# Performance work log

Measured on AMD Instinct MI355X. Metric: run time of the kernel, lower is better.

Reference implementation:

```python
import jax, jax.numpy as jnp
import numpy as np

TAU = 0.05
SIGMA = 0.05
THETA = 1.0
MAX_ITER = 30
B, N, M1, M2 = 8192, 256, 128, 64


def setup_inputs() -> dict:
    key = jax.random.key(0)
    k = jax.random.split(key, 5)
    x0 = jax.random.normal(k[0], (B, N), dtype=jnp.float32)
    y1_0 = jnp.zeros((B, M1), dtype=jnp.float32)
    y2_0 = jnp.zeros((B, M2), dtype=jnp.float32)
    z = jax.random.normal(k[1], (B, M1 + M2), dtype=jnp.float32)
    c = jax.random.normal(k[2], (N,), dtype=jnp.float32)
    # scale constraint matrices so tau*sigma*||A||^2 < 1 (PDHG stability)
    A1 = jax.random.normal(k[3], (M1, N), dtype=jnp.float32) * 0.1
    A2 = jax.random.normal(k[4], (M2, N), dtype=jnp.float32) * 0.1
    return {"x0": x0, "y1_0": y1_0, "y2_0": y2_0, "z": z, "c": c, "A1": A1, "A2": A2}


def reference(x0, y1_0, y2_0, z, c, A1, A2):
    # affine constraint maps: ineq_map(x, z) = x @ A1^T - z1 ; eq_map(x, z) = x @ A2^T - z2
    # adjoints: A1^T y1 = y1 @ A1 ; A2^T y2 = y2 @ A2
    # prox: projection onto nonnegative orthant
    z1, z2 = z[:, :M1], z[:, M1:]

    def step(carry, _):
        x, x_bar, y1, y2 = carry
        y1 = jnp.maximum(y1 + SIGMA * (x_bar @ A1.T - z1), 0.0)   # dual ineq ascent + clamp
        y2 = y2 + SIGMA * (x_bar @ A2.T - z2)                     # dual eq ascent
        grad = c + y1 @ A1 + y2 @ A2                              # [B, N] via broadcast of c
        x_next = jnp.maximum(x - TAU * grad, 0.0)                 # prox (nonneg projection)
        x_bar = x_next + THETA * (x_next - x)                     # extrapolation
        return (x_next, x_bar, y1, y2), None

    (x, _, y1, y2), _ = jax.lax.scan(step, (x0, x0, y1_0, y2_0), None, length=MAX_ITER)
    return (x, y1, y2)
```

## Files before the change

kernel.cpp:

```cpp
#include <hip/hip_runtime.h>

typedef __attribute__((ext_vector_type(8))) __bf16 bf16x8;
typedef __attribute__((ext_vector_type(4))) float f32x4;
typedef __attribute__((ext_vector_type(4))) int i32x4;

constexpr int Bn = 8192, Nn = 256, M1n = 128, M2n = 64, Mn = 192, ITERS = 30;
constexpr float TAUc = 0.05f, SIGc = 0.05f;

__device__ __forceinline__ ushort f2bf(float f) {
  unsigned u = __builtin_bit_cast(unsigned, f);
  u = (u + 0x7FFFu + ((u >> 16) & 1u)) >> 16;
  return (ushort)u;
}

__device__ __forceinline__ unsigned cvtpk(float lo, float hi) {
  unsigned r;
  asm("v_cvt_pk_bf16_f32 %0, %1, %2" : "=v"(r) : "v"(lo), "v"(hi));
  return r;
}

__device__ __forceinline__ void pina(i32x4& v) { asm volatile("" : "+a"(v)); }

__device__ __forceinline__ f32x4 mfma_swp(i32x4 afrag, bf16x8 b, f32x4 acc) {
  return __builtin_amdgcn_mfma_f32_16x16x32_bf16(
      __builtin_bit_cast(bf16x8, afrag), b, acc, 0, 0, 0);
}

__global__ void prep_kernel(const float* __restrict__ A1, const float* __restrict__ A2,
                            ushort* __restrict__ Arm, ushort* __restrict__ AT) {
  int i = blockIdx.x * 256 + threadIdx.x;
  if (i >= Mn * Nn) return;
  int m = i / Nn, n = i % Nn;
  float v = (m < M1n) ? A1[m * Nn + n] : A2[(m - M1n) * Nn + n];
  ushort b = f2bf(v);
  Arm[m * Nn + n] = b;
  AT[n * Mn + m] = b;
}

__global__ __launch_bounds__(512, 2) void pdhg_kernel(
    const float* __restrict__ x0, const float* __restrict__ y10,
    const float* __restrict__ y20, const float* __restrict__ z,
    const float* __restrict__ c, const ushort* __restrict__ Arm,
    const ushort* __restrict__ AT, float* __restrict__ out) {
  __shared__ __align__(16) ushort xb_lds[2][16][264];
  __shared__ __align__(16) ushort y_lds[2][16][200];

  const int lane = threadIdx.x & 63;
  const int w = threadIdx.x >> 6;
  const int fr = lane & 15;
  const int kg = lane >> 4;
  const int row0 = blockIdx.x * 32;

  const int b1 = w & 1;
  const int mg = w >> 1;
  const int rG1 = row0 + 16 * b1 + fr;

  float x[2][2][4];
  float cv[2][4];
  float ys[3][4], zs[3][4];

#pragma unroll
  for (int t = 0; t < 2; ++t) {
    const int n0 = (2 * w + t) * 16 + kg * 4;
    *reinterpret_cast<f32x4*>(cv[t]) = *reinterpret_cast<const f32x4*>(&c[n0]);
#pragma unroll
    for (int b = 0; b < 2; ++b) {
      f32x4 v = *reinterpret_cast<const f32x4*>(&x0[(row0 + 16 * b + fr) * Nn + n0]);
#pragma unroll
      for (int g = 0; g < 4; ++g) x[t][b][g] = v[g];
      uint2 p = make_uint2(cvtpk(v[0], v[1]), cvtpk(v[2], v[3]));
      *reinterpret_cast<uint2*>(&xb_lds[b][fr][n0]) = p;
    }
  }
#pragma unroll
  for (int i = 0; i < 3; ++i) {
    const int mt = 3 * mg + i;
    const int m0 = mt * 16 + kg * 4;
    f32x4 zv = *reinterpret_cast<const f32x4*>(&z[rG1 * Mn + m0]);
    f32x4 yv = (mt < 8) ? *reinterpret_cast<const f32x4*>(&y10[rG1 * M1n + m0])
                        : *reinterpret_cast<const f32x4*>(&y20[rG1 * M2n + (m0 - M1n)]);
#pragma unroll
    for (int g = 0; g < 4; ++g) { zs[i][g] = SIGc * zv[g]; ys[i][g] = yv[g]; }
  }

  i32x4 armF[3][8], atF[2][6];
#pragma unroll
  for (int i = 0; i < 3; ++i) {
    const int m = (3 * mg + i) * 16 + fr;
#pragma unroll
    for (int kf = 0; kf < 8; ++kf) {
      armF[i][kf] = *reinterpret_cast<const i32x4*>(&Arm[m * Nn + kf * 32 + kg * 8]);
      pina(armF[i][kf]);
    }
  }
#pragma unroll
  for (int t = 0; t < 2; ++t) {
    const int n = (2 * w + t) * 16 + fr;
#pragma unroll
    for (int kf = 0; kf < 6; ++kf) {
      atF[t][kf] = *reinterpret_cast<const i32x4*>(&AT[n * Mn + kf * 32 + kg * 8]);
      pina(atF[t][kf]);
    }
  }

  __syncthreads();

  for (int it = 0; it < ITERS; ++it) {
    f32x4 a0 = {0.f, 0.f, 0.f, 0.f}, a1 = a0, a2 = a0;
#pragma unroll
    for (int kf = 0; kf < 8; ++kf) {
      bf16x8 fx = *reinterpret_cast<const bf16x8*>(&xb_lds[b1][fr][kf * 32 + kg * 8]);
      a0 = mfma_swp(armF[0][kf], fx, a0);
      a1 = mfma_swp(armF[1][kf], fx, a1);
      a2 = mfma_swp(armF[2][kf], fx, a2);
    }

#pragma unroll
    for (int i = 0; i < 3; ++i) {
      const int mt = 3 * mg + i;
      const int m0 = mt * 16 + kg * 4;
      const f32x4 ai = (i == 0) ? a0 : (i == 1) ? a1 : a2;
      const bool relu = (mt < 8);
#pragma unroll
      for (int g = 0; g < 4; ++g) {
        float s = __builtin_fmaf(SIGc, ai[g], ys[i][g]) - zs[i][g];
        ys[i][g] = relu ? fmaxf(s, 0.f) : s;
      }
      uint2 p = make_uint2(cvtpk(ys[i][0], ys[i][1]), cvtpk(ys[i][2], ys[i][3]));
      *reinterpret_cast<uint2*>(&y_lds[b1][fr][m0]) = p;
    }
    __syncthreads();

    f32x4 q00 = {0.f, 0.f, 0.f, 0.f}, q01 = q00, q10 = q00, q11 = q00;
#pragma unroll
    for (int kf = 0; kf < 6; ++kf) {
      bf16x8 g0 = *reinterpret_cast<const bf16x8*>(&y_lds[0][fr][kf * 32 + kg * 8]);
      bf16x8 g1 = *reinterpret_cast<const bf16x8*>(&y_lds[1][fr][kf * 32 + kg * 8]);
      q00 = mfma_swp(atF[0][kf], g0, q00);
      q01 = mfma_swp(atF[1][kf], g0, q01);
      q10 = mfma_swp(atF[0][kf], g1, q10);
      q11 = mfma_swp(atF[1][kf], g1, q11);
    }

    const bool notlast = (it != ITERS - 1);
#pragma unroll
    for (int t = 0; t < 2; ++t) {
      const int n0 = (2 * w + t) * 16 + kg * 4;
#pragma unroll
      for (int b = 0; b < 2; ++b) {
        const f32x4 qt = (t == 0) ? (b == 0 ? q00 : q10) : (b == 0 ? q01 : q11);
        float xb[4];
#pragma unroll
        for (int g = 0; g < 4; ++g) {
          float grad = cv[t][g] + qt[g];
          float xn = fmaxf(__builtin_fmaf(-TAUc, grad, x[t][b][g]), 0.f);
          xb[g] = 2.f * xn - x[t][b][g];
          x[t][b][g] = xn;
        }
        if (notlast) {
          uint2 p = make_uint2(cvtpk(xb[0], xb[1]), cvtpk(xb[2], xb[3]));
          *reinterpret_cast<uint2*>(&xb_lds[b][fr][n0]) = p;
        }
      }
    }
    if (notlast) __syncthreads();
  }

  float* ox = out;
  float* oy1 = out + Bn * Nn;
  float* oy2 = oy1 + Bn * M1n;
#pragma unroll
  for (int t = 0; t < 2; ++t) {
    const int n0 = (2 * w + t) * 16 + kg * 4;
#pragma unroll
    for (int b = 0; b < 2; ++b) {
      f32x4 v;
#pragma unroll
      for (int g = 0; g < 4; ++g) v[g] = x[t][b][g];
      *reinterpret_cast<f32x4*>(&ox[(row0 + 16 * b + fr) * Nn + n0]) = v;
    }
  }
#pragma unroll
  for (int i = 0; i < 3; ++i) {
    const int mt = 3 * mg + i;
    const int m0 = mt * 16 + kg * 4;
    f32x4 v;
#pragma unroll
    for (int g = 0; g < 4; ++g) v[g] = ys[i][g];
    if (mt < 8) *reinterpret_cast<f32x4*>(&oy1[rG1 * M1n + m0]) = v;
    else        *reinterpret_cast<f32x4*>(&oy2[rG1 * M2n + (m0 - M1n)]) = v;
  }
}

extern "C" void kernel_launch(void* const* d_in, const int* in_sizes, int n_in,
                              void* d_out, int out_size, void* d_ws, size_t ws_size,
                              hipStream_t stream) {
  const float* x0  = (const float*)d_in[0];
  const float* y10 = (const float*)d_in[1];
  const float* y20 = (const float*)d_in[2];
  const float* z   = (const float*)d_in[3];
  const float* c   = (const float*)d_in[4];
  const float* A1  = (const float*)d_in[5];
  const float* A2  = (const float*)d_in[6];

  ushort* Arm = (ushort*)d_ws;
  ushort* AT  = Arm + Mn * Nn;

  prep_kernel<<<(Mn * Nn + 255) / 256, 256, 0, stream>>>(A1, A2, Arm, AT);
  pdhg_kernel<<<Bn / 32, 512, 0, stream>>>(x0, y10, y20, z, c, Arm, AT, (float*)d_out);
}
```

Before: 67.69 us.

## Shrink PDHG blocks to 16 rows with 4 waves each

```diff
diff --git a/kernel.cpp b/kernel.cpp
--- a/kernel.cpp
+++ b/kernel.cpp
@@ -37,56 +37,50 @@
   AT[n * Mn + m] = b;
 }
 
-__global__ __launch_bounds__(512, 2) void pdhg_kernel(
+__global__ __launch_bounds__(256, 2) void pdhg_kernel(
     const float* __restrict__ x0, const float* __restrict__ y10,
     const float* __restrict__ y20, const float* __restrict__ z,
     const float* __restrict__ c, const ushort* __restrict__ Arm,
     const ushort* __restrict__ AT, float* __restrict__ out) {
-  __shared__ __align__(16) ushort xb_lds[2][16][264];
-  __shared__ __align__(16) ushort y_lds[2][16][200];
+  __shared__ __align__(16) ushort xb_lds[16][264];
+  __shared__ __align__(16) ushort y_lds[16][200];
 
   const int lane = threadIdx.x & 63;
   const int w = threadIdx.x >> 6;
   const int fr = lane & 15;
   const int kg = lane >> 4;
-  const int row0 = blockIdx.x * 32;
+  const int row0 = blockIdx.x * 16;
+  const int rG = row0 + fr;
 
-  const int b1 = w & 1;
-  const int mg = w >> 1;
-  const int rG1 = row0 + 16 * b1 + fr;
-
-  float x[2][2][4];
-  float cv[2][4];
+  float x[4][4];
+  float cv[4][4];
   float ys[3][4], zs[3][4];
 
 #pragma unroll
-  for (int t = 0; t < 2; ++t) {
-    const int n0 = (2 * w + t) * 16 + kg * 4;
+  for (int t = 0; t < 4; ++t) {
+    const int n0 = (4 * w + t) * 16 + kg * 4;
     *reinterpret_cast<f32x4*>(cv[t]) = *reinterpret_cast<const f32x4*>(&c[n0]);
+    f32x4 v = *reinterpret_cast<const f32x4*>(&x0[rG * Nn + n0]);
 #pragma unroll
-    for (int b = 0; b < 2; ++b) {
-      f32x4 v = *reinterpret_cast<const f32x4*>(&x0[(row0 + 16 * b + fr) * Nn + n0]);
-#pragma unroll
-      for (int g = 0; g < 4; ++g) x[t][b][g] = v[g];
-      uint2 p = make_uint2(cvtpk(v[0], v[1]), cvtpk(v[2], v[3]));
-      *reinterpret_cast<uint2*>(&xb_lds[b][fr][n0]) = p;
-    }
+    for (int g = 0; g < 4; ++g) x[t][g] = v[g];
+    uint2 p = make_uint2(cvtpk(v[0], v[1]), cvtpk(v[2], v[3]));
+    *reinterpret_cast<uint2*>(&xb_lds[fr][n0]) = p;
   }
 #pragma unroll
   for (int i = 0; i < 3; ++i) {
-    const int mt = 3 * mg + i;
+    const int mt = 3 * w + i;
     const int m0 = mt * 16 + kg * 4;
-    f32x4 zv = *reinterpret_cast<const f32x4*>(&z[rG1 * Mn + m0]);
-    f32x4 yv = (mt < 8) ? *reinterpret_cast<const f32x4*>(&y10[rG1 * M1n + m0])
-                        : *reinterpret_cast<const f32x4*>(&y20[rG1 * M2n + (m0 - M1n)]);
+    f32x4 zv = *reinterpret_cast<const f32x4*>(&z[rG * Mn + m0]);
+    f32x4 yv = (mt < 8) ? *reinterpret_cast<const f32x4*>(&y10[rG * M1n + m0])
+                        : *reinterpret_cast<const f32x4*>(&y20[rG * M2n + (m0 - M1n)]);
 #pragma unroll
     for (int g = 0; g < 4; ++g) { zs[i][g] = SIGc * zv[g]; ys[i][g] = yv[g]; }
   }
 
-  i32x4 armF[3][8], atF[2][6];
+  i32x4 armF[3][8], atF[4][6];
 #pragma unroll
   for (int i = 0; i < 3; ++i) {
-    const int m = (3 * mg + i) * 16 + fr;
+    const int m = (3 * w + i) * 16 + fr;
 #pragma unroll
     for (int kf = 0; kf < 8; ++kf) {
       armF[i][kf] = *reinterpret_cast<const i32x4*>(&Arm[m * Nn + kf * 32 + kg * 8]);
@@ -94,8 +88,8 @@
     }
   }
 #pragma unroll
-  for (int t = 0; t < 2; ++t) {
-    const int n = (2 * w + t) * 16 + fr;
+  for (int t = 0; t < 4; ++t) {
+    const int n = (4 * w + t) * 16 + fr;
 #pragma unroll
     for (int kf = 0; kf < 6; ++kf) {
       atF[t][kf] = *reinterpret_cast<const i32x4*>(&AT[n * Mn + kf * 32 + kg * 8]);
@@ -109,7 +103,7 @@
     f32x4 a0 = {0.f, 0.f, 0.f, 0.f}, a1 = a0, a2 = a0;
 #pragma unroll
     for (int kf = 0; kf < 8; ++kf) {
-      bf16x8 fx = *reinterpret_cast<const bf16x8*>(&xb_lds[b1][fr][kf * 32 + kg * 8]);
+      bf16x8 fx = *reinterpret_cast<const bf16x8*>(&xb_lds[fr][kf * 32 + kg * 8]);
       a0 = mfma_swp(armF[0][kf], fx, a0);
       a1 = mfma_swp(armF[1][kf], fx, a1);
       a2 = mfma_swp(armF[2][kf], fx, a2);
@@ -117,7 +111,7 @@
 
 #pragma unroll
     for (int i = 0; i < 3; ++i) {
-      const int mt = 3 * mg + i;
+      const int mt = 3 * w + i;
       const int m0 = mt * 16 + kg * 4;
       const f32x4 ai = (i == 0) ? a0 : (i == 1) ? a1 : a2;
       const bool relu = (mt < 8);
@@ -127,40 +121,36 @@
         ys[i][g] = relu ? fmaxf(s, 0.f) : s;
       }
       uint2 p = make_uint2(cvtpk(ys[i][0], ys[i][1]), cvtpk(ys[i][2], ys[i][3]));
-      *reinterpret_cast<uint2*>(&y_lds[b1][fr][m0]) = p;
+      *reinterpret_cast<uint2*>(&y_lds[fr][m0]) = p;
     }
     __syncthreads();
 
-    f32x4 q00 = {0.f, 0.f, 0.f, 0.f}, q01 = q00, q10 = q00, q11 = q00;
+    f32x4 q0 = {0.f, 0.f, 0.f, 0.f}, q1 = q0, q2 = q0, q3 = q0;
 #pragma unroll
     for (int kf = 0; kf < 6; ++kf) {
-      bf16x8 g0 = *reinterpret_cast<const bf16x8*>(&y_lds[0][fr][kf * 32 + kg * 8]);
-      bf16x8 g1 = *reinterpret_cast<const bf16x8*>(&y_lds[1][fr][kf * 32 + kg * 8]);
-      q00 = mfma_swp(atF[0][kf], g0, q00);
-      q01 = mfma_swp(atF[1][kf], g0, q01);
-      q10 = mfma_swp(atF[0][kf], g1, q10);
-      q11 = mfma_swp(atF[1][kf], g1, q11);
+      bf16x8 fy = *reinterpret_cast<const bf16x8*>(&y_lds[fr][kf * 32 + kg * 8]);
+      q0 = mfma_swp(atF[0][kf], fy, q0);
+      q1 = mfma_swp(atF[1][kf], fy, q1);
+      q2 = mfma_swp(atF[2][kf], fy, q2);
+      q3 = mfma_swp(atF[3][kf], fy, q3);
     }
 
     const bool notlast = (it != ITERS - 1);
 #pragma unroll
-    for (int t = 0; t < 2; ++t) {
-      const int n0 = (2 * w + t) * 16 + kg * 4;
+    for (int t = 0; t < 4; ++t) {
+      const int n0 = (4 * w + t) * 16 + kg * 4;
+      const f32x4 qt = (t == 0) ? q0 : (t == 1) ? q1 : (t == 2) ? q2 : q3;
+      float xb[4];
 #pragma unroll
-      for (int b = 0; b < 2; ++b) {
-        const f32x4 qt = (t == 0) ? (b == 0 ? q00 : q10) : (b == 0 ? q01 : q11);
-        float xb[4];
-#pragma unroll
-        for (int g = 0; g < 4; ++g) {
-          float grad = cv[t][g] + qt[g];
-          float xn = fmaxf(__builtin_fmaf(-TAUc, grad, x[t][b][g]), 0.f);
-          xb[g] = 2.f * xn - x[t][b][g];
-          x[t][b][g] = xn;
-        }
-        if (notlast) {
-          uint2 p = make_uint2(cvtpk(xb[0], xb[1]), cvtpk(xb[2], xb[3]));
-          *reinterpret_cast<uint2*>(&xb_lds[b][fr][n0]) = p;
-        }
+      for (int g = 0; g < 4; ++g) {
+        float grad = cv[t][g] + qt[g];
+        float xn = fmaxf(__builtin_fmaf(-TAUc, grad, x[t][g]), 0.f);
+        xb[g] = 2.f * xn - x[t][g];
+        x[t][g] = xn;
+      }
+      if (notlast) {
+        uint2 p = make_uint2(cvtpk(xb[0], xb[1]), cvtpk(xb[2], xb[3]));
+        *reinterpret_cast<uint2*>(&xb_lds[fr][n0]) = p;
       }
     }
     if (notlast) __syncthreads();
@@ -170,25 +160,22 @@
   float* oy1 = out + Bn * Nn;
   float* oy2 = oy1 + Bn * M1n;
 #pragma unroll
-  for (int t = 0; t < 2; ++t) {
-    const int n0 = (2 * w + t) * 16 + kg * 4;
+  for (int t = 0; t < 4; ++t) {
+    const int n0 = (4 * w + t) * 16 + kg * 4;
+    f32x4 v;
 #pragma unroll
-    for (int b = 0; b < 2; ++b) {
-      f32x4 v;
-#pragma unroll
-      for (int g = 0; g < 4; ++g) v[g] = x[t][b][g];
-      *reinterpret_cast<f32x4*>(&ox[(row0 + 16 * b + fr) * Nn + n0]) = v;
-    }
+    for (int g = 0; g < 4; ++g) v[g] = x[t][g];
+    *reinterpret_cast<f32x4*>(&ox[rG * Nn + n0]) = v;
   }
 #pragma unroll
   for (int i = 0; i < 3; ++i) {
-    const int mt = 3 * mg + i;
+    const int mt = 3 * w + i;
     const int m0 = mt * 16 + kg * 4;
     f32x4 v;
 #pragma unroll
     for (int g = 0; g < 4; ++g) v[g] = ys[i][g];
-    if (mt < 8) *reinterpret_cast<f32x4*>(&oy1[rG1 * M1n + m0]) = v;
-    else        *reinterpret_cast<f32x4*>(&oy2[rG1 * M2n + (m0 - M1n)]) = v;
+    if (mt < 8) *reinterpret_cast<f32x4*>(&oy1[rG * M1n + m0]) = v;
+    else        *reinterpret_cast<f32x4*>(&oy2[rG * M2n + (m0 - M1n)]) = v;
   }
 }
 
@@ -207,5 +194,5 @@
   ushort* AT  = Arm + Mn * Nn;
 
   prep_kernel<<<(Mn * Nn + 255) / 256, 256, 0, stream>>>(A1, A2, Arm, AT);
-  pdhg_kernel<<<Bn / 32, 512, 0, stream>>>(x0, y10, y20, z, c, Arm, AT, (float*)d_out);
+  pdhg_kernel<<<Bn / 16, 256, 0, stream>>>(x0, y10, y20, z, c, Arm, AT, (float*)d_out);
 }
```

After: 102.2 us. 1.51x slower.

## Software-pipeline the two 16-row halves so dual and primal GEMMs overlap

Applied to the files above, without the earlier changes.

```diff
diff --git a/kernel.cpp b/kernel.cpp
--- a/kernel.cpp
+++ b/kernel.cpp
@@ -51,13 +51,16 @@
   const int kg = lane >> 4;
   const int row0 = blockIdx.x * 32;
 
-  const int b1 = w & 1;
-  const int mg = w >> 1;
-  const int rG1 = row0 + 16 * b1 + fr;
+  const bool heavy = (w < 4);
+  const int mt0 = heavy ? 2 * w : 4 + w;
+  const int mt1 = 2 * w + 1;
+  const int m00 = mt0 * 16 + kg * 4;
+  const int m01 = mt1 * 16 + kg * 4;
 
   float x[2][2][4];
   float cv[2][4];
-  float ys[3][4], zs[3][4];
+  float ys[2][2][4];
+  float zs[2][2][4];
 
 #pragma unroll
   for (int t = 0; t < 2; ++t) {
@@ -67,30 +70,40 @@
     for (int b = 0; b < 2; ++b) {
       f32x4 v = *reinterpret_cast<const f32x4*>(&x0[(row0 + 16 * b + fr) * Nn + n0]);
 #pragma unroll
-      for (int g = 0; g < 4; ++g) x[t][b][g] = v[g];
+      for (int g = 0; g < 4; ++g) x[b][t][g] = v[g];
       uint2 p = make_uint2(cvtpk(v[0], v[1]), cvtpk(v[2], v[3]));
       *reinterpret_cast<uint2*>(&xb_lds[b][fr][n0]) = p;
     }
   }
 #pragma unroll
-  for (int i = 0; i < 3; ++i) {
-    const int mt = 3 * mg + i;
-    const int m0 = mt * 16 + kg * 4;
-    f32x4 zv = *reinterpret_cast<const f32x4*>(&z[rG1 * Mn + m0]);
-    f32x4 yv = (mt < 8) ? *reinterpret_cast<const f32x4*>(&y10[rG1 * M1n + m0])
-                        : *reinterpret_cast<const f32x4*>(&y20[rG1 * M2n + (m0 - M1n)]);
-#pragma unroll
-    for (int g = 0; g < 4; ++g) { zs[i][g] = SIGc * zv[g]; ys[i][g] = yv[g]; }
-  }
-
-  i32x4 armF[3][8], atF[2][6];
-#pragma unroll
-  for (int i = 0; i < 3; ++i) {
-    const int m = (3 * mg + i) * 16 + fr;
+  for (int b = 0; b < 2; ++b) {
+    const int rGb = row0 + 16 * b + fr;
+    {
+      f32x4 zv = *reinterpret_cast<const f32x4*>(&z[rGb * Mn + m00]);
+      f32x4 yv = heavy ? *reinterpret_cast<const f32x4*>(&y10[rGb * M1n + m00])
+                       : *reinterpret_cast<const f32x4*>(&y20[rGb * M2n + (m00 - M1n)]);
+#pragma unroll
+      for (int g = 0; g < 4; ++g) { zs[b][0][g] = SIGc * zv[g]; ys[b][0][g] = yv[g]; }
+    }
+    if (heavy) {
+      f32x4 zv = *reinterpret_cast<const f32x4*>(&z[rGb * Mn + m01]);
+      f32x4 yv = *reinterpret_cast<const f32x4*>(&y10[rGb * M1n + m01]);
+#pragma unroll
+      for (int g = 0; g < 4; ++g) { zs[b][1][g] = SIGc * zv[g]; ys[b][1][g] = yv[g]; }
+    }
+  }
+
+  i32x4 armF[2][8], atF[2][6];
+#pragma unroll
+  for (int kf = 0; kf < 8; ++kf) {
+    armF[0][kf] = *reinterpret_cast<const i32x4*>(&Arm[(mt0 * 16 + fr) * Nn + kf * 32 + kg * 8]);
+    pina(armF[0][kf]);
+  }
+  if (heavy) {
 #pragma unroll
     for (int kf = 0; kf < 8; ++kf) {
-      armF[i][kf] = *reinterpret_cast<const i32x4*>(&Arm[m * Nn + kf * 32 + kg * 8]);
-      pina(armF[i][kf]);
+      armF[1][kf] = *reinterpret_cast<const i32x4*>(&Arm[(mt1 * 16 + fr) * Nn + kf * 32 + kg * 8]);
+      pina(armF[1][kf]);
     }
   }
 #pragma unroll
@@ -103,92 +116,108 @@
     }
   }
 
-  __syncthreads();
-
-  for (int it = 0; it < ITERS; ++it) {
-    f32x4 a0 = {0.f, 0.f, 0.f, 0.f}, a1 = a0, a2 = a0;
-#pragma unroll
-    for (int kf = 0; kf < 8; ++kf) {
-      bf16x8 fx = *reinterpret_cast<const bf16x8*>(&xb_lds[b1][fr][kf * 32 + kg * 8]);
-      a0 = mfma_swp(armF[0][kf], fx, a0);
-      a1 = mfma_swp(armF[1][kf], fx, a1);
-      a2 = mfma_swp(armF[2][kf], fx, a2);
-    }
-
-#pragma unroll
-    for (int i = 0; i < 3; ++i) {
-      const int mt = 3 * mg + i;
-      const int m0 = mt * 16 + kg * 4;
-      const f32x4 ai = (i == 0) ? a0 : (i == 1) ? a1 : a2;
-      const bool relu = (mt < 8);
+  auto do_g1 = [&](int b) {
+    f32x4 h0 = {0.f, 0.f, 0.f, 0.f}, h1 = h0;
+    if (heavy) {
+#pragma unroll
+      for (int kf = 0; kf < 8; ++kf) {
+        bf16x8 fx = *reinterpret_cast<const bf16x8*>(&xb_lds[b][fr][kf * 32 + kg * 8]);
+        h0 = mfma_swp(armF[0][kf], fx, h0);
+        h1 = mfma_swp(armF[1][kf], fx, h1);
+      }
+    } else {
+#pragma unroll
+      for (int kf = 0; kf < 8; ++kf) {
+        bf16x8 fx = *reinterpret_cast<const bf16x8*>(&xb_lds[b][fr][kf * 32 + kg * 8]);
+        h0 = mfma_swp(armF[0][kf], fx, h0);
+      }
+    }
+#pragma unroll
+    for (int g = 0; g < 4; ++g) {
+      float s = __builtin_fmaf(SIGc, h0[g], ys[b][0][g]) - zs[b][0][g];
+      ys[b][0][g] = heavy ? fmaxf(s, 0.f) : s;
+    }
+    {
+      uint2 p = make_uint2(cvtpk(ys[b][0][0], ys[b][0][1]), cvtpk(ys[b][0][2], ys[b][0][3]));
+      *reinterpret_cast<uint2*>(&y_lds[b][fr][m00]) = p;
+    }
+    if (heavy) {
 #pragma unroll
       for (int g = 0; g < 4; ++g) {
-        float s = __builtin_fmaf(SIGc, ai[g], ys[i][g]) - zs[i][g];
-        ys[i][g] = relu ? fmaxf(s, 0.f) : s;
-      }
-      uint2 p = make_uint2(cvtpk(ys[i][0], ys[i][1]), cvtpk(ys[i][2], ys[i][3]));
-      *reinterpret_cast<uint2*>(&y_lds[b1][fr][m0]) = p;
-    }
-    __syncthreads();
-
-    f32x4 q00 = {0.f, 0.f, 0.f, 0.f}, q01 = q00, q10 = q00, q11 = q00;
+        float s = __builtin_fmaf(SIGc, h1[g], ys[b][1][g]) - zs[b][1][g];
+        ys[b][1][g] = fmaxf(s, 0.f);
+      }
+      uint2 p = make_uint2(cvtpk(ys[b][1][0], ys[b][1][1]), cvtpk(ys[b][1][2], ys[b][1][3]));
+      *reinterpret_cast<uint2*>(&y_lds[b][fr][m01]) = p;
+    }
+  };
+
+  auto do_g3 = [&](int b) {
+    f32x4 q0 = {0.f, 0.f, 0.f, 0.f}, q1 = q0;
 #pragma unroll
     for (int kf = 0; kf < 6; ++kf) {
-      bf16x8 g0 = *reinterpret_cast<const bf16x8*>(&y_lds[0][fr][kf * 32 + kg * 8]);
-      bf16x8 g1 = *reinterpret_cast<const bf16x8*>(&y_lds[1][fr][kf * 32 + kg * 8]);
-      q00 = mfma_swp(atF[0][kf], g0, q00);
-      q01 = mfma_swp(atF[1][kf], g0, q01);
-      q10 = mfma_swp(atF[0][kf], g1, q10);
-      q11 = mfma_swp(atF[1][kf], g1, q11);
-    }
-
-    const bool notlast = (it != ITERS - 1);
+      bf16x8 fy = *reinterpret_cast<const bf16x8*>(&y_lds[b][fr][kf * 32 + kg * 8]);
+      q0 = mfma_swp(atF[0][kf], fy, q0);
+      q1 = mfma_swp(atF[1][kf], fy, q1);
+    }
 #pragma unroll
     for (int t = 0; t < 2; ++t) {
       const int n0 = (2 * w + t) * 16 + kg * 4;
-#pragma unroll
-      for (int b = 0; b < 2; ++b) {
-        const f32x4 qt = (t == 0) ? (b == 0 ? q00 : q10) : (b == 0 ? q01 : q11);
-        float xb[4];
-#pragma unroll
-        for (int g = 0; g < 4; ++g) {
-          float grad = cv[t][g] + qt[g];
-          float xn = fmaxf(__builtin_fmaf(-TAUc, grad, x[t][b][g]), 0.f);
-          xb[g] = 2.f * xn - x[t][b][g];
-          x[t][b][g] = xn;
-        }
-        if (notlast) {
-          uint2 p = make_uint2(cvtpk(xb[0], xb[1]), cvtpk(xb[2], xb[3]));
-          *reinterpret_cast<uint2*>(&xb_lds[b][fr][n0]) = p;
-        }
-      }
-    }
-    if (notlast) __syncthreads();
+      const f32x4 qt = t ? q1 : q0;
+      float xb[4];
+#pragma unroll
+      for (int g = 0; g < 4; ++g) {
+        float grad = cv[t][g] + qt[g];
+        float xn = fmaxf(__builtin_fmaf(-TAUc, grad, x[b][t][g]), 0.f);
+        xb[g] = 2.f * xn - x[b][t][g];
+        x[b][t][g] = xn;
+      }
+      uint2 p = make_uint2(cvtpk(xb[0], xb[1]), cvtpk(xb[2], xb[3]));
+      *reinterpret_cast<uint2*>(&xb_lds[b][fr][n0]) = p;
+    }
+  };
+
+  __syncthreads();
+
+  do_g1(1);
+  __syncthreads();
+
+  for (int it = 1; it <= ITERS; ++it) {
+    do_g1(0);
+    do_g3(1);
+    __syncthreads();
+    if (it < ITERS) do_g1(1);
+    do_g3(0);
+    if (it < ITERS) __syncthreads();
   }
 
   float* ox = out;
   float* oy1 = out + Bn * Nn;
   float* oy2 = oy1 + Bn * M1n;
 #pragma unroll
-  for (int t = 0; t < 2; ++t) {
-    const int n0 = (2 * w + t) * 16 + kg * 4;
-#pragma unroll
-    for (int b = 0; b < 2; ++b) {
+  for (int b = 0; b < 2; ++b) {
+    const int rGb = row0 + 16 * b + fr;
+#pragma unroll
+    for (int t = 0; t < 2; ++t) {
+      const int n0 = (2 * w + t) * 16 + kg * 4;
       f32x4 v;
 #pragma unroll
-      for (int g = 0; g < 4; ++g) v[g] = x[t][b][g];
-      *reinterpret_cast<f32x4*>(&ox[(row0 + 16 * b + fr) * Nn + n0]) = v;
-    }
-  }
-#pragma unroll
-  for (int i = 0; i < 3; ++i) {
-    const int mt = 3 * mg + i;
-    const int m0 = mt * 16 + kg * 4;
-    f32x4 v;
-#pragma unroll
-    for (int g = 0; g < 4; ++g) v[g] = ys[i][g];
-    if (mt < 8) *reinterpret_cast<f32x4*>(&oy1[rG1 * M1n + m0]) = v;
-    else        *reinterpret_cast<f32x4*>(&oy2[rG1 * M2n + (m0 - M1n)]) = v;
+      for (int g = 0; g < 4; ++g) v[g] = x[b][t][g];
+      *reinterpret_cast<f32x4*>(&ox[rGb * Nn + n0]) = v;
+    }
+    {
+      f32x4 v;
+#pragma unroll
+      for (int g = 0; g < 4; ++g) v[g] = ys[b][0][g];
+      if (heavy) *reinterpret_cast<f32x4*>(&oy1[rGb * M1n + m00]) = v;
+      else       *reinterpret_cast<f32x4*>(&oy2[rGb * M2n + (m00 - M1n)]) = v;
+    }
+    if (heavy) {
+      f32x4 v;
+#pragma unroll
+      for (int g = 0; g < 4; ++g) v[g] = ys[b][1][g];
+      *reinterpret_cast<f32x4*>(&oy1[rGb * M1n + m01]) = v;
+    }
   }
 }
 
```

Result: slower. 72.87 us (+7.6%).
